# Performance work log

Measured on AMD Instinct MI355X. Metric: run time of the kernel, lower is better.

## Reference

```python
import jax, jax.numpy as jnp
import numpy as np
import math

D_MODEL = 1024
D_STATE = 128
EXPAND = 2
HEADDIM = 64
NGROUPS = 1
ROPE_FRACTION = 0.5
A_FLOOR = 1e-4
D_INNER = EXPAND * D_MODEL            # 2048
NHEADS = D_INNER // HEADDIM           # 32
SPLIT = int(D_STATE * ROPE_FRACTION)  # 64
R = SPLIT // 2                        # 32 rotary angles; rotary applied to first R state dims
D_IN_PROJ = 2 * D_INNER + 2 * D_STATE * NGROUPS + 3 * NHEADS + R  # 4480
BATCH = 1
SEQLEN = 1024


def setup_inputs() -> dict:
    key = jax.random.key(0)
    k0, k1, k2, k3 = jax.random.split(key, 4)
    u = jax.random.normal(k0, (BATCH, SEQLEN, D_MODEL), jnp.float32)
    w_in = jax.random.normal(k1, (D_IN_PROJ, D_MODEL), jnp.float32) * (D_MODEL ** -0.5)
    w_out = jax.random.normal(k2, (D_MODEL, D_INNER), jnp.float32) * (D_INNER ** -0.5)
    # dt_bias init matches torch: inverse-softplus of dt ~ LogUniform(dt_min, dt_max)
    dt = jnp.exp(jax.random.uniform(k3, (NHEADS,), jnp.float32)
                 * (math.log(0.1) - math.log(0.001)) + math.log(0.001))
    dt = jnp.maximum(dt, 1e-4)
    dt_bias = dt + jnp.log(-jnp.expm1(-dt))
    D = jnp.ones((NHEADS,), jnp.float32)
    return {"u": u, "w_in": w_in, "w_out": w_out, "dt_bias": dt_bias, "D": D}


def _mamba3_forward(u, w_in, w_out, dt_bias, D):
    b, l, _ = u.shape
    proj = u @ w_in.T  # [b, l, D_IN_PROJ]
    sizes = [D_INNER, D_INNER, D_STATE * NGROUPS, D_STATE * NGROUPS, NHEADS, NHEADS, NHEADS, R]
    idx = np.cumsum(sizes)[:-1]
    z, x, B, C, dd_dt, dd_A, trap, angles = jnp.split(proj, idx, axis=-1)

    A = jnp.minimum(-jax.nn.softplus(dd_A), -A_FLOOR)      # [b,l,h]
    dt = jax.nn.softplus(dd_dt + dt_bias)                  # [b,l,h]
    tr = jax.nn.sigmoid(trap)                              # [b,l,h]
    # rotary angle: tanh(angles)[b,l,1,R] * dt[b,l,h,1] * pi, cumsum over time
    theta = jnp.cumsum(jnp.tanh(angles)[:, :, None, :] * dt[..., None] * jnp.pi, axis=1)  # [b,l,h,R]

    x_h = x.reshape(b, l, NHEADS, HEADDIM)
    z_h = z.reshape(b, l, NHEADS, HEADDIM)
    B_h = B.reshape(b, l, NGROUPS, D_STATE)[:, :, 0, :]  # only group 0 is read in the loop
    C_h = C.reshape(b, l, NGROUPS, D_STATE)[:, :, 0, :]

    def step(carry, inp):
        sr, si, px = carry  # sr: [b,h,p,n], si: [b,h,p,R] (imag beyond R is identically zero)
        dt_t, A_t, tr_t, th, bt, ct, xt = inp
        alpha = jnp.exp(A_t * dt_t)[:, :, None, None]          # [b,h,1,1]
        beta = ((1.0 - tr_t) * dt_t)[:, :, None, None] * alpha
        gamma = (tr_t * dt_t)[:, :, None, None]
        base = bt[:, None, None, :] * (px[..., None] * beta + xt[..., None] * gamma)  # [b,h,p,n]
        rc = jnp.cos(th)[:, :, None, :]  # [b,h,1,R]
        rs = jnp.sin(th)[:, :, None, :]
        sr = sr * alpha + jnp.concatenate([base[..., :R] * rc, base[..., R:]], axis=-1)
        si = si * alpha + base[..., :R] * rs
        ctb = ct[:, None, None, :]
        y = (jnp.sum((sr[..., :R] * rc + si * rs) * ctb[..., :R], axis=-1)
             + jnp.sum(sr[..., R:] * ctb[..., R:], axis=-1))  # [b,h,p]
        return (sr, si, xt), y

    sr0 = jnp.zeros((b, NHEADS, HEADDIM, D_STATE), u.dtype)
    si0 = jnp.zeros((b, NHEADS, HEADDIM, R), u.dtype)
    px0 = jnp.zeros((b, NHEADS, HEADDIM), u.dtype)
    xs = (jnp.moveaxis(dt, 1, 0), jnp.moveaxis(A, 1, 0), jnp.moveaxis(tr, 1, 0),
          jnp.moveaxis(theta, 1, 0), jnp.moveaxis(B_h, 1, 0), jnp.moveaxis(C_h, 1, 0),
          jnp.moveaxis(x_h, 1, 0))
    _, ys = jax.lax.scan(step, (sr0, si0, px0), xs)  # [l,b,h,p]
    y = jnp.moveaxis(ys, 0, 1) + D[None, None, :, None] * x_h
    out = y * jax.nn.silu(z_h)
    return out.reshape(b, l, D_INNER) @ w_out.T


def reference(u, w_in, w_out, dt_bias, D):
    return _mamba3_forward(u, w_in, w_out, dt_bias, D)
```

## Files before the change

kernel.cpp:

```cpp
#include <hip/hip_runtime.h>
#include <math.h>

#define L_SEQ   1024
#define DMODEL  1024
#define DINNER  2048
#define NH      32
#define HD      64
#define NS      160
#define RR      32
#define NPROJ   4480
#define OFF_Z   0
#define OFF_X   2048
#define OFF_B   4096
#define OFF_C   4224
#define OFF_DT  4352
#define OFF_A   4384
#define OFF_TR  4416
#define OFF_ANG 4448
#define NC      16
#define CL      64
#define PIF     3.14159265358979323846f

typedef __attribute__((ext_vector_type(8))) short bf16x8;
typedef __attribute__((ext_vector_type(4))) float f32x4;
typedef unsigned int u32;
typedef unsigned short u16;

__device__ __forceinline__ float softplusf(float x) {
  return (x > 20.f) ? x : log1pf(expf(x));
}
__device__ __forceinline__ u16 f2bf(float f) {
  u32 u = __float_as_uint(f);
  u32 r = (u + 0x7FFFu + ((u >> 16) & 1u)) >> 16;
  return (u16)r;
}
__device__ __forceinline__ float bf2f(u16 v) {
  return __uint_as_float(((u32)v) << 16);
}

__device__ __forceinline__ void gload_lds16(const u16* g, u16* l) {
  __builtin_amdgcn_global_load_lds(
      (const __attribute__((address_space(1))) u32*)(unsigned long long)(const void*)g,
      (__attribute__((address_space(3))) u32*)(unsigned long long)(void*)l, 16, 0, 0);
}

__global__ __launch_bounds__(256) void cvt2_bf16(
    const float* __restrict__ s0, u16* __restrict__ d0, int q0,
    const float* __restrict__ s1, u16* __restrict__ d1, int q1) {
  int i = blockIdx.x * 256 + threadIdx.x;
  const float* s; u16* d; int j;
  if (i < q0) { s = s0; d = d0; j = i; }
  else { j = i - q0; if (j >= q1) return; s = s1; d = d1; }
  const float4* s4 = (const float4*)s;
  float4 a = s4[2 * j], b = s4[2 * j + 1];
  union { u16 h[8]; uint4 v; } o;
  o.h[0] = f2bf(a.x); o.h[1] = f2bf(a.y); o.h[2] = f2bf(a.z); o.h[3] = f2bf(a.w);
  o.h[4] = f2bf(b.x); o.h[5] = f2bf(b.y); o.h[6] = f2bf(b.z); o.h[7] = f2bf(b.w);
  ((uint4*)d)[j] = o.v;
}

template <int BM, int BN>
__global__ __launch_bounds__(256) void gemm_bf16(
    const u16* __restrict__ A, const u16* __restrict__ B,
    float* __restrict__ C, int N, int K) {
  constexpr int BK = 32;
  constexpr int WM = BM / 2, WN = BN / 2;
  constexpr int MF = WM / 16, NF = WN / 16;
  constexpr int CA = BM / 64;
  constexpr int CB = BN / 64;
  __shared__ u16 lds[(BM + BN) * BK];

  const int bm = blockIdx.y * BM, bn = blockIdx.x * BN;
  const int tid = threadIdx.x, w = tid >> 6, lane = tid & 63;
  const int wr = w >> 1, wc = w & 1;
  const int fr = lane & 15, sl = lane >> 4;
  const int lrow = lane >> 2, lslot = (lane & 3) * 8;

  const u16* gA[CA]; u16* lA[CA];
#pragma unroll
  for (int j = 0; j < CA; ++j) {
    int ca = w * CA + j;
    gA[j] = A + (size_t)(bm + ca * 16 + lrow) * K + lslot;
    lA[j] = lds + ca * 512;
  }
  const u16* gB[CB]; u16* lB[CB];
#pragma unroll
  for (int j = 0; j < CB; ++j) {
    int cb = w * CB + j;
    gB[j] = B + (size_t)(bn + cb * 16 + lrow) * K + lslot;
    lB[j] = lds + BM * 32 + cb * 512;
  }

  const u16* aptr[MF]; const u16* bptr[NF];
#pragma unroll
  for (int i = 0; i < MF; ++i)
    aptr[i] = lds + (wr * WM + i * 16 + fr) * 32 + sl * 8;
#pragma unroll
  for (int j = 0; j < NF; ++j)
    bptr[j] = lds + BM * 32 + (wc * WN + j * 16 + fr) * 32 + sl * 8;

  f32x4 acc[MF][NF] = {};
  const int iters = K / BK;

#pragma unroll
  for (int j = 0; j < CA; ++j) gload_lds16(gA[j], lA[j]);
#pragma unroll
  for (int j = 0; j < CB; ++j) gload_lds16(gB[j], lB[j]);

  for (int it = 0; it < iters; ++it) {
    __syncthreads();
    bf16x8 af[MF], bfv[NF];
#pragma unroll
    for (int i = 0; i < MF; ++i) af[i] = *(const bf16x8*)aptr[i];
#pragma unroll
    for (int j = 0; j < NF; ++j) bfv[j] = *(const bf16x8*)bptr[j];
    __syncthreads();
    if (it + 1 < iters) {
#pragma unroll
      for (int j = 0; j < CA; ++j) gload_lds16(gA[j] + (it + 1) * BK, lA[j]);
#pragma unroll
      for (int j = 0; j < CB; ++j) gload_lds16(gB[j] + (it + 1) * BK, lB[j]);
    }
#pragma unroll
    for (int i = 0; i < MF; ++i)
#pragma unroll
      for (int j = 0; j < NF; ++j)
        acc[i][j] = __builtin_amdgcn_mfma_f32_16x16x32_bf16(
            af[i], bfv[j], acc[i][j], 0, 0, 0);
  }

#pragma unroll
  for (int i = 0; i < MF; ++i) {
    int rb = bm + wr * WM + i * 16 + sl * 4;
#pragma unroll
    for (int j = 0; j < NF; ++j) {
      int cb = bn + wc * WN + j * 16 + fr;
#pragma unroll
      for (int r = 0; r < 4; ++r)
        C[(size_t)(rb + r) * N + cb] = acc[i][j][r];
    }
  }
}

__global__ __launch_bounds__(256) void prep_scalars_cvt(
    const float* __restrict__ proj, const float* __restrict__ dt_bias,
    float* __restrict__ dtA, float* __restrict__ lnaA,
    float* __restrict__ betaA, float* __restrict__ gammaA,
    float* __restrict__ angP,
    const float* __restrict__ wsrc, u16* __restrict__ wdst) {
  const int b = blockIdx.x;
  if (b < 1024) {
    int j = b * 256 + threadIdx.x;
    const float4* s4 = (const float4*)wsrc;
    float4 a = s4[2 * j], bb = s4[2 * j + 1];
    union { u16 h[8]; uint4 v; } o;
    o.h[0] = f2bf(a.x); o.h[1] = f2bf(a.y); o.h[2] = f2bf(a.z); o.h[3] = f2bf(a.w);
    o.h[4] = f2bf(bb.x); o.h[5] = f2bf(bb.y); o.h[6] = f2bf(bb.z); o.h[7] = f2bf(bb.w);
    ((uint4*)wdst)[j] = o.v;
    return;
  }
  int idx = (b - 1024) * 256 + threadIdx.x;
  int h = idx & 31, l = idx >> 5;
  const float* prow = proj + (size_t)l * NPROJ;
  float dt = softplusf(prow[OFF_DT + h] + dt_bias[h]);
  float Apos = fmaxf(softplusf(prow[OFF_A + h]), 1e-4f);
  float tr = 1.f / (1.f + expf(-prow[OFF_TR + h]));
  float lna = -Apos * dt;
  float alpha = expf(lna);
  dtA[idx] = dt;
  lnaA[idx] = lna;
  betaA[idx] = (1.f - tr) * dt * alpha;
  gammaA[idx] = tr * dt;
  angP[idx] = tanhf(prow[OFF_ANG + h]) * PIF;
}

__global__ __launch_bounds__(256) void theta_scan(
    const float* __restrict__ angP, const float* __restrict__ dtA,
    float* __restrict__ rc, float* __restrict__ rs) {
  const int h = blockIdx.x >> 5;
  const int r = blockIdx.x & 31;
  const int tid = threadIdx.x;
  __shared__ float ldssc[256];

  float csum[4];
  float run = 0.f;
#pragma unroll
  for (int i = 0; i < 4; ++i) {
    int l = tid * 4 + i;
    run += angP[l * NH + r] * dtA[l * NH + h];
    csum[i] = run;
  }
  ldssc[tid] = run;
  __syncthreads();
  for (int off = 1; off < 256; off <<= 1) {
    float t = (tid >= off) ? ldssc[tid - off] : 0.f;
    __syncthreads();
    ldssc[tid] += t;
    __syncthreads();
  }
  float excl = ldssc[tid] - run;
#pragma unroll
  for (int i = 0; i < 4; ++i) {
    int l = tid * 4 + i;
    float th = excl + csum[i];
    size_t o = ((size_t)l * NH + h) * RR + r;
    rc[o] = cosf(th);
    rs[o] = sinf(th);
  }
}

__global__ __launch_bounds__(256) void uvgA(
    const float* __restrict__ proj, const float* __restrict__ betaA,
    const float* __restrict__ gammaA, const float* __restrict__ lnaA,
    const float* __restrict__ rc, const float* __restrict__ rs,
    u16* __restrict__ U, u16* __restrict__ V, u16* __restrict__ Gt,
    float* __restrict__ cumA, float* __restrict__ adec,
    u16* __restrict__ S) {
  const int h = blockIdx.x >> 4, c = blockIdx.x & 15;
  const int c0 = c * CL;
  const int tid = threadIdx.x;
  const int w = tid >> 6, lane = tid & 63;

  __shared__ __attribute__((aligned(16))) char smem[54784];
  u16 (*Gw)[72]   = (u16(*)[72])(smem);
  float* wsc      = (float*)(smem + 9216);
  float* bet      = (float*)(smem + 9472);
  float* gam      = (float*)(smem + 9728);
  float (*xs)[64] = (float(*)[64])(smem + 10240);
  u16 (*Vl)[168]  = (u16(*)[168])(smem + 10240);
  u16 (*Vt)[72]   = (u16(*)[72])(smem + 31744);

  if (w < 3) {
    for (int i = tid; i < 65 * 16; i += 192) {
      int r = i >> 4, c4 = i & 15;
      int l = c0 - 1 + r;
      float4 v = {0.f, 0.f, 0.f, 0.f};
      if (l >= 0)
        v = *(const float4*)(proj + (size_t)l * NPROJ + OFF_X + h * HD + c4 * 4);
      *(float4*)&xs[r][c4 * 4] = v;
    }
  } else {
    const int t = lane;
    float v = lnaA[(c0 + t) * NH + h];
#pragma unroll
    for (int k = 1; k < 64; k <<= 1) {
      int src = t - k;
      float o = __shfl(v, src < 0 ? 0 : src);
      if (t >= k) v += o;
    }
    cumA[(size_t)h * L_SEQ + c0 + t] = v;
    if (t == 63) adec[h * NC + c] = expf(v);
    float c63 = __shfl(v, 63);
    wsc[t] = expf(c63 - v);
    bet[t] = betaA[(c0 + t) * NH + h];
    gam[t] = gammaA[(c0 + t) * NH + h];
  }
  __syncthreads();

  {
    const int p = lane;
    union { u16 hh[16]; uint4 q[2]; } og, ow;
    float xprev = xs[w * 16][p];
#pragma unroll
    for (int i = 0; i < 16; ++i) {
      int s = w * 16 + i;
      float xcur = xs[s + 1][p];
      float g = bet[s] * xprev + gam[s] * xcur;
      og.hh[i] = f2bf(g);
      ow.hh[i] = f2bf(g * wsc[s]);
      xprev = xcur;
    }
    uint4* gdst = (uint4*)(Gt + (((size_t)h * NC + c) * HD + p) * CL + w * 16);
    gdst[0] = og.q[0];
    gdst[1] = og.q[1];
    *(uint4*)&Gw[p][w * 16] = ow.q[0];
    *(uint4*)&Gw[p][w * 16 + 8] = ow.q[1];
  }
  __syncthreads();

  if (tid < 160) {
    const int n = tid;
    const int idxB = (n < 64) ? (n & 31) : (n - 32);
    const bool is_re = (n < 32);
    const bool has_rot = (n < 64);
    for (int ss = 0; ss < 64; ++ss) {
      int l = c0 + ss;
      const float* prow = proj + (size_t)l * NPROJ;
      float Bv = prow[OFF_B + idxB];
      float Cv = prow[OFF_C + idxB];
      if (has_rot) {
        float rv = is_re ? rc[((size_t)l * NH + h) * RR + idxB]
                         : rs[((size_t)l * NH + h) * RR + idxB];
        Bv *= rv; Cv *= rv;
      }
      u16 bb = f2bf(Bv);
      U[((size_t)h * L_SEQ + l) * NS + n] = f2bf(Cv);
      V[((size_t)h * L_SEQ + l) * NS + n] = bb;
      Vl[ss][n] = bb;
    }
  }
  __syncthreads();

  if (tid < 160) {
    int n = tid;
#pragma unroll
    for (int s2 = 0; s2 < 32; ++s2) {
      u32 lo = Vl[2 * s2][n], hi = Vl[2 * s2 + 1][n];
      *(u32*)&Vt[n][2 * s2] = lo | (hi << 16);
    }
  }
  __syncthreads();

  const int wr = w >> 1, wc = w & 1;
  const int fr = lane & 15, sl = lane >> 4;
  f32x4 acc[2][5] = {};
#pragma unroll
  for (int ks = 0; ks < 2; ++ks) {
    bf16x8 a0 = *(const bf16x8*)&Gw[wr * 32 + fr][ks * 32 + sl * 8];
    bf16x8 a1 = *(const bf16x8*)&Gw[wr * 32 + 16 + fr][ks * 32 + sl * 8];
    bf16x8 bv[5];
#pragma unroll
    for (int fj = 0; fj < 5; ++fj)
      bv[fj] = *(const bf16x8*)&Vt[wc * 80 + fj * 16 + fr][ks * 32 + sl * 8];
#pragma unroll
    for (int fj = 0; fj < 5; ++fj) {
      acc[0][fj] = __builtin_amdgcn_mfma_f32_16x16x32_bf16(a0, bv[fj], acc[0][fj], 0, 0, 0);
      acc[1][fj] = __builtin_amdgcn_mfma_f32_16x16x32_bf16(a1, bv[fj], acc[1][fj], 0, 0, 0);
    }
  }
  u16* Fb = S + (size_t)(c * NH + h) * HD * NS;
#pragma unroll
  for (int fi = 0; fi < 2; ++fi)
#pragma unroll
    for (int fj = 0; fj < 5; ++fj)
#pragma unroll
      for (int r = 0; r < 4; ++r) {
        int p = wr * 32 + fi * 16 + sl * 4 + r;
        int n = wc * 80 + fj * 16 + fr;
        Fb[(size_t)p * NS + n] = f2bf(acc[fi][fj][r]);
      }
}

__global__ __launch_bounds__(256) void combine(
    u16* __restrict__ S, const float* __restrict__ adec) {
  const int idx = blockIdx.x * 256 + threadIdx.x;
  if (idx >= NH * HD * NS) return;
  const int n = idx % NS;
  const int rem = idx / NS;
  const int p = rem & 63;
  const int h = rem >> 6;
  float F = 0.f;
  for (int c = 0; c < NC; ++c) {
    size_t off = ((size_t)(c * NH + h) * HD + p) * NS + n;
    float sv = bf2f(S[off]);
    S[off] = f2bf(F);
    F = fmaf(F, adec[h * NC + c], sv);
  }
}

__global__ __launch_bounds__(256) void passB(
    const float* __restrict__ proj, const u16* __restrict__ U,
    const u16* __restrict__ V, const u16* __restrict__ Gt,
    const float* __restrict__ cumA, const u16* __restrict__ S,
    const float* __restrict__ Dvec, u16* __restrict__ yz) {
  const int c = blockIdx.x >> 5, h = blockIdx.x & 31;
  const int c0 = c * CL;
  const int tid = threadIdx.x;
  const int w = tid >> 6, lane = tid & 63;
  const int wr = w >> 1, wc = w & 1;
  const int fr = lane & 15, sl = lane >> 4;
  __shared__ u16 Ul[64][168];
  __shared__ u16 BB[64][168];
  __shared__ u16 Ml[64][72];
  __shared__ u16 Gl[64][72];
  __shared__ float cums[64], ecum[64];

  const u16* Us = U + ((size_t)h * L_SEQ + c0) * NS;
  for (int i = tid; i < 1280; i += 256) {
    int r = i / 20, ch = i % 20;
    *(uint4*)&Ul[r][ch * 8] = *(const uint4*)(Us + (size_t)r * NS + ch * 8);
  }
  {
    const u16* S0 = S + (size_t)(c * NH + h) * HD * NS;
    for (int i = tid; i < 1280; i += 256) {
      int r = i / 20, ch = i % 20;
      *(uint4*)&BB[r][ch * 8] = *(const uint4*)(S0 + (size_t)r * NS + ch * 8);
    }
  }
  if (tid < 64) {
    float cv = cumA[(size_t)h * L_SEQ + c0 + tid];
    cums[tid] = cv;
    ecum[tid] = expf(cv);
  }
  __syncthreads();

  f32x4 acc[2][2] = {};
#pragma unroll
  for (int ks = 0; ks < 5; ++ks) {
    bf16x8 a0 = *(const bf16x8*)&Ul[wr * 32 + fr][ks * 32 + sl * 8];
    bf16x8 a1 = *(const bf16x8*)&Ul[wr * 32 + 16 + fr][ks * 32 + sl * 8];
    bf16x8 b0 = *(const bf16x8*)&BB[wc * 32 + fr][ks * 32 + sl * 8];
    bf16x8 b1 = *(const bf16x8*)&BB[wc * 32 + 16 + fr][ks * 32 + sl * 8];
    acc[0][0] = __builtin_amdgcn_mfma_f32_16x16x32_bf16(a0, b0, acc[0][0], 0, 0, 0);
    acc[0][1] = __builtin_amdgcn_mfma_f32_16x16x32_bf16(a0, b1, acc[0][1], 0, 0, 0);
    acc[1][0] = __builtin_amdgcn_mfma_f32_16x16x32_bf16(a1, b0, acc[1][0], 0, 0, 0);
    acc[1][1] = __builtin_amdgcn_mfma_f32_16x16x32_bf16(a1, b1, acc[1][1], 0, 0, 0);
  }
#pragma unroll
  for (int fi = 0; fi < 2; ++fi)
#pragma unroll
    for (int fj = 0; fj < 2; ++fj)
#pragma unroll
      for (int r = 0; r < 4; ++r)
        acc[fi][fj][r] *= ecum[wr * 32 + fi * 16 + sl * 4 + r];
  __syncthreads();

  const u16* Vs = V + ((size_t)h * L_SEQ + c0) * NS;
  for (int i = tid; i < 1280; i += 256) {
    int r = i / 20, ch = i % 20;
    *(uint4*)&BB[r][ch * 8] = *(const uint4*)(Vs + (size_t)r * NS + ch * 8);
  }
  const u16* Gs = Gt + ((size_t)h * NC + c) * HD * CL;
  for (int i = tid; i < 512; i += 256) {
    int p = i >> 3, ch = i & 7;
    *(uint4*)&Gl[p][ch * 8] = *(const uint4*)(Gs + (size_t)p * CL + ch * 8);
  }
  __syncthreads();

  f32x4 pac[2][2] = {};
#pragma unroll
  for (int ks = 0; ks < 5; ++ks) {
    bf16x8 a0 = *(const bf16x8*)&Ul[wr * 32 + fr][ks * 32 + sl * 8];
    bf16x8 a1 = *(const bf16x8*)&Ul[wr * 32 + 16 + fr][ks * 32 + sl * 8];
    bf16x8 b0 = *(const bf16x8*)&BB[wc * 32 + fr][ks * 32 + sl * 8];
    bf16x8 b1 = *(const bf16x8*)&BB[wc * 32 + 16 + fr][ks * 32 + sl * 8];
    pac[0][0] = __builtin_amdgcn_mfma_f32_16x16x32_bf16(a0, b0, pac[0][0], 0, 0, 0);
    pac[0][1] = __builtin_amdgcn_mfma_f32_16x16x32_bf16(a0, b1, pac[0][1], 0, 0, 0);
    pac[1][0] = __builtin_amdgcn_mfma_f32_16x16x32_bf16(a1, b0, pac[1][0], 0, 0, 0);
    pac[1][1] = __builtin_amdgcn_mfma_f32_16x16x32_bf16(a1, b1, pac[1][1], 0, 0, 0);
  }
#pragma unroll
  for (int fi = 0; fi < 2; ++fi)
#pragma unroll
    for (int fj = 0; fj < 2; ++fj)
#pragma unroll
      for (int r = 0; r < 4; ++r) {
        int t = wr * 32 + fi * 16 + sl * 4 + r;
        int ss = wc * 32 + fj * 16 + fr;
        float m = (ss <= t) ? expf(cums[t] - cums[ss]) * pac[fi][fj][r] : 0.f;
        Ml[t][ss] = f2bf(m);
      }
  __syncthreads();

#pragma unroll
  for (int ks = 0; ks < 2; ++ks) {
    bf16x8 a0 = *(const bf16x8*)&Ml[wr * 32 + fr][ks * 32 + sl * 8];
    bf16x8 a1 = *(const bf16x8*)&Ml[wr * 32 + 16 + fr][ks * 32 + sl * 8];
    bf16x8 b0 = *(const bf16x8*)&Gl[wc * 32 + fr][ks * 32 + sl * 8];
    bf16x8 b1 = *(const bf16x8*)&Gl[wc * 32 + 16 + fr][ks * 32 + sl * 8];
    acc[0][0] = __builtin_amdgcn_mfma_f32_16x16x32_bf16(a0, b0, acc[0][0], 0, 0, 0);
    acc[0][1] = __builtin_amdgcn_mfma_f32_16x16x32_bf16(a0, b1, acc[0][1], 0, 0, 0);
    acc[1][0] = __builtin_amdgcn_mfma_f32_16x16x32_bf16(a1, b0, acc[1][0], 0, 0, 0);
    acc[1][1] = __builtin_amdgcn_mfma_f32_16x16x32_bf16(a1, b1, acc[1][1], 0, 0, 0);
  }

  const float Dh = Dvec[h];
#pragma unroll
  for (int fi = 0; fi < 2; ++fi)
#pragma unroll
    for (int fj = 0; fj < 2; ++fj)
#pragma unroll
      for (int r = 0; r < 4; ++r) {
        int t = wr * 32 + fi * 16 + sl * 4 + r;
        int p = wc * 32 + fj * 16 + fr;
        int l = c0 + t;
        float x = proj[(size_t)l * NPROJ + OFF_X + h * HD + p];
        float z = proj[(size_t)l * NPROJ + OFF_Z + h * HD + p];
        float y = acc[fi][fj][r] + Dh * x;
        float sg = z / (1.f + expf(-z));
        yz[(size_t)l * DINNER + h * HD + p] = f2bf(y * sg);
      }
}

extern "C" void kernel_launch(void* const* d_in, const int* in_sizes, int n_in,
                              void* d_out, int out_size, void* d_ws, size_t ws_size,
                              hipStream_t stream) {
  const float* u       = (const float*)d_in[0];
  const float* w_in    = (const float*)d_in[1];
  const float* w_out   = (const float*)d_in[2];
  const float* dt_bias = (const float*)d_in[3];
  const float* Dvec    = (const float*)d_in[4];
  float* out = (float*)d_out;

  float* ws = (float*)d_ws;
  float* proj   = ws;
  float* dtA    = proj + 4587520;
  float* lnaA   = dtA + 32768;
  float* betaA  = lnaA + 32768;
  float* gammaA = betaA + 32768;
  float* cumA   = gammaA + 32768;
  float* adec   = cumA + 32768;
  float* angP   = adec + 512;
  float* rcb    = angP + 32768;
  float* rsb    = rcb + 1048576;
  u16*   Sb     = (u16*)(rsb + 1048576);
  u16*   Gtb    = Sb + 5242880;
  u16*   Ubuf   = Gtb + 2097152;
  u16*   Vbuf   = Ubuf + 5242880;
  u16*   yzb    = Vbuf + 5242880;
  u16*   wob    = yzb + 2097152;
  u16*   ub     = Ubuf;
  u16*   wib    = Ubuf + 1048576;

  cvt2_bf16<<<(131072 + 573440) / 256, 256, 0, stream>>>(
      u, ub, 131072, w_in, wib, 573440);

  gemm_bf16<128, 128><<<dim3(NPROJ / 128, L_SEQ / 128), 256, 0, stream>>>(
      ub, wib, proj, NPROJ, DMODEL);

  prep_scalars_cvt<<<1024 + 128, 256, 0, stream>>>(
      proj, dt_bias, dtA, lnaA, betaA, gammaA, angP, w_out, wob);

  theta_scan<<<NH * RR, 256, 0, stream>>>(angP, dtA, rcb, rsb);

  uvgA<<<NH * NC, 256, 0, stream>>>(
      proj, betaA, gammaA, lnaA, rcb, rsb, Ubuf, Vbuf, Gtb, cumA, adec, Sb);

  combine<<<(NH * HD * NS + 255) / 256, 256, 0, stream>>>(Sb, adec);

  passB<<<NC * NH, 256, 0, stream>>>(
      proj, Ubuf, Vbuf, Gtb, cumA, Sb, Dvec, yzb);

  gemm_bf16<64, 64><<<dim3(DMODEL / 64, L_SEQ / 64), 256, 0, stream>>>(
      yzb, wob, out, DMODEL, DINNER);
}
```

Before: 133.9 us.

## Fuse scan pipeline into one persistent kernel with software grid barriers

Merges prep_scalars, theta_scan, uvgA, combine and passB into a single 512-block persistent kernel separated by atomic-based grid barriers. The w_out bf16 conversion moves into the initial conversion kernel, and the bf16 copies of u and w_in are relocated into the S buffer. This removes several kernel launch gaps and tail effects. The cost is barrier spin overhead, and correctness depends on all 512 blocks being co-resident, which launch_bounds(256,2) is meant to help.

```diff
diff --git a/kernel.cpp b/kernel.cpp
--- a/kernel.cpp
+++ b/kernel.cpp
@@ -44,13 +44,34 @@
       (__attribute__((address_space(3))) u32*)(unsigned long long)(void*)l, 16, 0, 0);
 }
 
-__global__ __launch_bounds__(256) void cvt2_bf16(
-    const float* __restrict__ s0, u16* __restrict__ d0, int q0,
-    const float* __restrict__ s1, u16* __restrict__ d1, int q1) {
+__device__ __forceinline__ void grid_bar(u32* bar) {
+  __syncthreads();
+  if (threadIdx.x == 0) {
+    __threadfence();
+    u32 gen = __hip_atomic_load(bar + 1, __ATOMIC_RELAXED, __HIP_MEMORY_SCOPE_AGENT);
+    u32 arr = __hip_atomic_fetch_add(bar, 1u, __ATOMIC_ACQ_REL, __HIP_MEMORY_SCOPE_AGENT);
+    if (arr + 1u == gridDim.x) {
+      __hip_atomic_store(bar, 0u, __ATOMIC_RELAXED, __HIP_MEMORY_SCOPE_AGENT);
+      __hip_atomic_store(bar + 1, gen + 1u, __ATOMIC_RELEASE, __HIP_MEMORY_SCOPE_AGENT);
+    } else {
+      while (__hip_atomic_load(bar + 1, __ATOMIC_ACQUIRE, __HIP_MEMORY_SCOPE_AGENT) == gen)
+        __builtin_amdgcn_s_sleep(2);
+    }
+    __threadfence();
+  }
+  __syncthreads();
+}
+
+__global__ __launch_bounds__(256) void cvt3(
+    const float* __restrict__ s0, u16* __restrict__ d0,
+    const float* __restrict__ s1, u16* __restrict__ d1,
+    const float* __restrict__ s2, u16* __restrict__ d2) {
   int i = blockIdx.x * 256 + threadIdx.x;
   const float* s; u16* d; int j;
-  if (i < q0) { s = s0; d = d0; j = i; }
-  else { j = i - q0; if (j >= q1) return; s = s1; d = d1; }
+  if (i < 131072)      { s = s0; d = d0; j = i; }
+  else if (i < 704512) { s = s1; d = d1; j = i - 131072; }
+  else if (i < 966656) { s = s2; d = d2; j = i - 704512; }
+  else return;
   const float4* s4 = (const float4*)s;
   float4 a = s4[2 * j], b = s4[2 * j + 1];
   union { u16 h[8]; uint4 v; } o;
@@ -142,344 +163,329 @@
   }
 }
 
-__global__ __launch_bounds__(256) void prep_scalars_cvt(
+__global__ __launch_bounds__(256, 2) void mega(
     const float* __restrict__ proj, const float* __restrict__ dt_bias,
+    const float* __restrict__ Dvec,
     float* __restrict__ dtA, float* __restrict__ lnaA,
     float* __restrict__ betaA, float* __restrict__ gammaA,
-    float* __restrict__ angP,
-    const float* __restrict__ wsrc, u16* __restrict__ wdst) {
-  const int b = blockIdx.x;
-  if (b < 1024) {
-    int j = b * 256 + threadIdx.x;
-    const float4* s4 = (const float4*)wsrc;
-    float4 a = s4[2 * j], bb = s4[2 * j + 1];
-    union { u16 h[8]; uint4 v; } o;
-    o.h[0] = f2bf(a.x); o.h[1] = f2bf(a.y); o.h[2] = f2bf(a.z); o.h[3] = f2bf(a.w);
-    o.h[4] = f2bf(bb.x); o.h[5] = f2bf(bb.y); o.h[6] = f2bf(bb.z); o.h[7] = f2bf(bb.w);
-    ((uint4*)wdst)[j] = o.v;
-    return;
-  }
-  int idx = (b - 1024) * 256 + threadIdx.x;
-  int h = idx & 31, l = idx >> 5;
-  const float* prow = proj + (size_t)l * NPROJ;
-  float dt = softplusf(prow[OFF_DT + h] + dt_bias[h]);
-  float Apos = fmaxf(softplusf(prow[OFF_A + h]), 1e-4f);
-  float tr = 1.f / (1.f + expf(-prow[OFF_TR + h]));
-  float lna = -Apos * dt;
-  float alpha = expf(lna);
-  dtA[idx] = dt;
-  lnaA[idx] = lna;
-  betaA[idx] = (1.f - tr) * dt * alpha;
-  gammaA[idx] = tr * dt;
-  angP[idx] = tanhf(prow[OFF_ANG + h]) * PIF;
-}
-
-__global__ __launch_bounds__(256) void theta_scan(
-    const float* __restrict__ angP, const float* __restrict__ dtA,
-    float* __restrict__ rc, float* __restrict__ rs) {
-  const int h = blockIdx.x >> 5;
-  const int r = blockIdx.x & 31;
-  const int tid = threadIdx.x;
-  __shared__ float ldssc[256];
-
-  float csum[4];
-  float run = 0.f;
-#pragma unroll
-  for (int i = 0; i < 4; ++i) {
-    int l = tid * 4 + i;
-    run += angP[l * NH + r] * dtA[l * NH + h];
-    csum[i] = run;
-  }
-  ldssc[tid] = run;
-  __syncthreads();
-  for (int off = 1; off < 256; off <<= 1) {
-    float t = (tid >= off) ? ldssc[tid - off] : 0.f;
-    __syncthreads();
-    ldssc[tid] += t;
-    __syncthreads();
-  }
-  float excl = ldssc[tid] - run;
-#pragma unroll
-  for (int i = 0; i < 4; ++i) {
-    int l = tid * 4 + i;
-    float th = excl + csum[i];
-    size_t o = ((size_t)l * NH + h) * RR + r;
-    rc[o] = cosf(th);
-    rs[o] = sinf(th);
-  }
-}
-
-__global__ __launch_bounds__(256) void uvgA(
-    const float* __restrict__ proj, const float* __restrict__ betaA,
-    const float* __restrict__ gammaA, const float* __restrict__ lnaA,
-    const float* __restrict__ rc, const float* __restrict__ rs,
-    u16* __restrict__ U, u16* __restrict__ V, u16* __restrict__ Gt,
     float* __restrict__ cumA, float* __restrict__ adec,
-    u16* __restrict__ S) {
-  const int h = blockIdx.x >> 4, c = blockIdx.x & 15;
-  const int c0 = c * CL;
-  const int tid = threadIdx.x;
-  const int w = tid >> 6, lane = tid & 63;
-
-  __shared__ __attribute__((aligned(16))) char smem[54784];
-  u16 (*Gw)[72]   = (u16(*)[72])(smem);
-  float* wsc      = (float*)(smem + 9216);
-  float* bet      = (float*)(smem + 9472);
-  float* gam      = (float*)(smem + 9728);
-  float (*xs)[64] = (float(*)[64])(smem + 10240);
-  u16 (*Vl)[168]  = (u16(*)[168])(smem + 10240);
-  u16 (*Vt)[72]   = (u16(*)[72])(smem + 31744);
-
-  if (w < 3) {
-    for (int i = tid; i < 65 * 16; i += 192) {
-      int r = i >> 4, c4 = i & 15;
-      int l = c0 - 1 + r;
-      float4 v = {0.f, 0.f, 0.f, 0.f};
-      if (l >= 0)
-        v = *(const float4*)(proj + (size_t)l * NPROJ + OFF_X + h * HD + c4 * 4);
-      *(float4*)&xs[r][c4 * 4] = v;
-    }
-  } else {
-    const int t = lane;
-    float v = lnaA[(c0 + t) * NH + h];
-#pragma unroll
-    for (int k = 1; k < 64; k <<= 1) {
-      int src = t - k;
-      float o = __shfl(v, src < 0 ? 0 : src);
-      if (t >= k) v += o;
-    }
-    cumA[(size_t)h * L_SEQ + c0 + t] = v;
-    if (t == 63) adec[h * NC + c] = expf(v);
-    float c63 = __shfl(v, 63);
-    wsc[t] = expf(c63 - v);
-    bet[t] = betaA[(c0 + t) * NH + h];
-    gam[t] = gammaA[(c0 + t) * NH + h];
-  }
-  __syncthreads();
-
-  {
-    const int p = lane;
-    union { u16 hh[16]; uint4 q[2]; } og, ow;
-    float xprev = xs[w * 16][p];
-#pragma unroll
-    for (int i = 0; i < 16; ++i) {
-      int s = w * 16 + i;
-      float xcur = xs[s + 1][p];
-      float g = bet[s] * xprev + gam[s] * xcur;
-      og.hh[i] = f2bf(g);
-      ow.hh[i] = f2bf(g * wsc[s]);
-      xprev = xcur;
-    }
-    uint4* gdst = (uint4*)(Gt + (((size_t)h * NC + c) * HD + p) * CL + w * 16);
-    gdst[0] = og.q[0];
-    gdst[1] = og.q[1];
-    *(uint4*)&Gw[p][w * 16] = ow.q[0];
-    *(uint4*)&Gw[p][w * 16 + 8] = ow.q[1];
-  }
-  __syncthreads();
-
-  if (tid < 160) {
-    const int n = tid;
-    const int idxB = (n < 64) ? (n & 31) : (n - 32);
-    const bool is_re = (n < 32);
-    const bool has_rot = (n < 64);
-    for (int ss = 0; ss < 64; ++ss) {
-      int l = c0 + ss;
-      const float* prow = proj + (size_t)l * NPROJ;
-      float Bv = prow[OFF_B + idxB];
-      float Cv = prow[OFF_C + idxB];
-      if (has_rot) {
-        float rv = is_re ? rc[((size_t)l * NH + h) * RR + idxB]
-                         : rs[((size_t)l * NH + h) * RR + idxB];
-        Bv *= rv; Cv *= rv;
-      }
-      u16 bb = f2bf(Bv);
-      U[((size_t)h * L_SEQ + l) * NS + n] = f2bf(Cv);
-      V[((size_t)h * L_SEQ + l) * NS + n] = bb;
-      Vl[ss][n] = bb;
-    }
-  }
-  __syncthreads();
-
-  if (tid < 160) {
-    int n = tid;
-#pragma unroll
-    for (int s2 = 0; s2 < 32; ++s2) {
-      u32 lo = Vl[2 * s2][n], hi = Vl[2 * s2 + 1][n];
-      *(u32*)&Vt[n][2 * s2] = lo | (hi << 16);
-    }
-  }
-  __syncthreads();
-
-  const int wr = w >> 1, wc = w & 1;
-  const int fr = lane & 15, sl = lane >> 4;
-  f32x4 acc[2][5] = {};
-#pragma unroll
-  for (int ks = 0; ks < 2; ++ks) {
-    bf16x8 a0 = *(const bf16x8*)&Gw[wr * 32 + fr][ks * 32 + sl * 8];
-    bf16x8 a1 = *(const bf16x8*)&Gw[wr * 32 + 16 + fr][ks * 32 + sl * 8];
-    bf16x8 bv[5];
-#pragma unroll
-    for (int fj = 0; fj < 5; ++fj)
-      bv[fj] = *(const bf16x8*)&Vt[wc * 80 + fj * 16 + fr][ks * 32 + sl * 8];
-#pragma unroll
-    for (int fj = 0; fj < 5; ++fj) {
-      acc[0][fj] = __builtin_amdgcn_mfma_f32_16x16x32_bf16(a0, bv[fj], acc[0][fj], 0, 0, 0);
-      acc[1][fj] = __builtin_amdgcn_mfma_f32_16x16x32_bf16(a1, bv[fj], acc[1][fj], 0, 0, 0);
-    }
-  }
-  u16* Fb = S + (size_t)(c * NH + h) * HD * NS;
-#pragma unroll
-  for (int fi = 0; fi < 2; ++fi)
-#pragma unroll
-    for (int fj = 0; fj < 5; ++fj)
-#pragma unroll
-      for (int r = 0; r < 4; ++r) {
-        int p = wr * 32 + fi * 16 + sl * 4 + r;
-        int n = wc * 80 + fj * 16 + fr;
-        Fb[(size_t)p * NS + n] = f2bf(acc[fi][fj][r]);
-      }
-}
-
-__global__ __launch_bounds__(256) void combine(
-    u16* __restrict__ S, const float* __restrict__ adec) {
-  const int idx = blockIdx.x * 256 + threadIdx.x;
-  if (idx >= NH * HD * NS) return;
-  const int n = idx % NS;
-  const int rem = idx / NS;
-  const int p = rem & 63;
-  const int h = rem >> 6;
-  float F = 0.f;
-  for (int c = 0; c < NC; ++c) {
-    size_t off = ((size_t)(c * NH + h) * HD + p) * NS + n;
-    float sv = bf2f(S[off]);
-    S[off] = f2bf(F);
-    F = fmaf(F, adec[h * NC + c], sv);
-  }
-}
-
-__global__ __launch_bounds__(256) void passB(
-    const float* __restrict__ proj, const u16* __restrict__ U,
-    const u16* __restrict__ V, const u16* __restrict__ Gt,
-    const float* __restrict__ cumA, const u16* __restrict__ S,
-    const float* __restrict__ Dvec, u16* __restrict__ yz) {
-  const int c = blockIdx.x >> 5, h = blockIdx.x & 31;
-  const int c0 = c * CL;
+    float* __restrict__ angP, float* __restrict__ rcb, float* __restrict__ rsb,
+    u16* __restrict__ Sb, u16* __restrict__ Gtb,
+    u16* __restrict__ Ubuf, u16* __restrict__ Vbuf,
+    u16* __restrict__ yzb, u32* bar) {
+  const int bid = blockIdx.x;
   const int tid = threadIdx.x;
   const int w = tid >> 6, lane = tid & 63;
   const int wr = w >> 1, wc = w & 1;
   const int fr = lane & 15, sl = lane >> 4;
-  __shared__ u16 Ul[64][168];
-  __shared__ u16 BB[64][168];
-  __shared__ u16 Ml[64][72];
-  __shared__ u16 Gl[64][72];
-  __shared__ float cums[64], ecum[64];
-
-  const u16* Us = U + ((size_t)h * L_SEQ + c0) * NS;
-  for (int i = tid; i < 1280; i += 256) {
-    int r = i / 20, ch = i % 20;
-    *(uint4*)&Ul[r][ch * 8] = *(const uint4*)(Us + (size_t)r * NS + ch * 8);
-  }
+
+  __shared__ __attribute__((aligned(16))) char smem[61952];
+
+  if (tid < 64) {
+    int idx = bid * 64 + tid;
+    int h = idx & 31, l = idx >> 5;
+    const float* prow = proj + (size_t)l * NPROJ;
+    float dt = softplusf(prow[OFF_DT + h] + dt_bias[h]);
+    float Apos = fmaxf(softplusf(prow[OFF_A + h]), 1e-4f);
+    float tr = 1.f / (1.f + expf(-prow[OFF_TR + h]));
+    float lna = -Apos * dt;
+    float alpha = expf(lna);
+    dtA[idx] = dt;
+    lnaA[idx] = lna;
+    betaA[idx] = (1.f - tr) * dt * alpha;
+    gammaA[idx] = tr * dt;
+    angP[idx] = tanhf(prow[OFF_ANG + h]) * PIF;
+  }
+  grid_bar(bar);
+
   {
-    const u16* S0 = S + (size_t)(c * NH + h) * HD * NS;
+    float* ldssc = (float*)smem;
+    for (int cc = 0; cc < 2; ++cc) {
+      int ch = bid * 2 + cc;
+      int h = ch >> 5, r = ch & 31;
+      float csum[4];
+      float run = 0.f;
+#pragma unroll
+      for (int i = 0; i < 4; ++i) {
+        int l = tid * 4 + i;
+        run += angP[l * NH + r] * dtA[l * NH + h];
+        csum[i] = run;
+      }
+      ldssc[tid] = run;
+      __syncthreads();
+      for (int off = 1; off < 256; off <<= 1) {
+        float t = (tid >= off) ? ldssc[tid - off] : 0.f;
+        __syncthreads();
+        ldssc[tid] += t;
+        __syncthreads();
+      }
+      float excl = ldssc[tid] - run;
+#pragma unroll
+      for (int i = 0; i < 4; ++i) {
+        int l = tid * 4 + i;
+        float th = excl + csum[i];
+        size_t o = ((size_t)l * NH + h) * RR + r;
+        rcb[o] = cosf(th);
+        rsb[o] = sinf(th);
+      }
+      __syncthreads();
+    }
+  }
+  grid_bar(bar);
+
+  {
+    const int h = bid >> 4, c = bid & 15;
+    const int c0 = c * CL;
+    u16 (*Gw)[72]   = (u16(*)[72])(smem);
+    float* wsc      = (float*)(smem + 9216);
+    float* bet      = (float*)(smem + 9472);
+    float* gam      = (float*)(smem + 9728);
+    float (*xs)[64] = (float(*)[64])(smem + 10240);
+    u16 (*Vl)[168]  = (u16(*)[168])(smem + 10240);
+    u16 (*Vt)[72]   = (u16(*)[72])(smem + 31744);
+
+    if (w < 3) {
+      for (int i = tid; i < 65 * 16; i += 192) {
+        int r = i >> 4, c4 = i & 15;
+        int l = c0 - 1 + r;
+        float4 v = {0.f, 0.f, 0.f, 0.f};
+        if (l >= 0)
+          v = *(const float4*)(proj + (size_t)l * NPROJ + OFF_X + h * HD + c4 * 4);
+        *(float4*)&xs[r][c4 * 4] = v;
+      }
+    } else {
+      const int t = lane;
+      float v = lnaA[(c0 + t) * NH + h];
+#pragma unroll
+      for (int k = 1; k < 64; k <<= 1) {
+        int src = t - k;
+        float o = __shfl(v, src < 0 ? 0 : src);
+        if (t >= k) v += o;
+      }
+      cumA[(size_t)h * L_SEQ + c0 + t] = v;
+      if (t == 63) adec[h * NC + c] = expf(v);
+      float c63 = __shfl(v, 63);
+      wsc[t] = expf(c63 - v);
+      bet[t] = betaA[(c0 + t) * NH + h];
+      gam[t] = gammaA[(c0 + t) * NH + h];
+    }
+    __syncthreads();
+
+    {
+      const int p = lane;
+      union { u16 hh[16]; uint4 q[2]; } og, ow;
+      float xprev = xs[w * 16][p];
+#pragma unroll
+      for (int i = 0; i < 16; ++i) {
+        int s = w * 16 + i;
+        float xcur = xs[s + 1][p];
+        float g = bet[s] * xprev + gam[s] * xcur;
+        og.hh[i] = f2bf(g);
+        ow.hh[i] = f2bf(g * wsc[s]);
+        xprev = xcur;
+      }
+      uint4* gdst = (uint4*)(Gtb + (((size_t)h * NC + c) * HD + p) * CL + w * 16);
+      gdst[0] = og.q[0];
+      gdst[1] = og.q[1];
+      *(uint4*)&Gw[p][w * 16] = ow.q[0];
+      *(uint4*)&Gw[p][w * 16 + 8] = ow.q[1];
+    }
+    __syncthreads();
+
+    if (tid < 160) {
+      const int n = tid;
+      const int idxB = (n < 64) ? (n & 31) : (n - 32);
+      const bool is_re = (n < 32);
+      const bool has_rot = (n < 64);
+      for (int ss = 0; ss < 64; ++ss) {
+        int l = c0 + ss;
+        const float* prow = proj + (size_t)l * NPROJ;
+        float Bv = prow[OFF_B + idxB];
+        float Cv = prow[OFF_C + idxB];
+        if (has_rot) {
+          float rv = is_re ? rcb[((size_t)l * NH + h) * RR + idxB]
+                           : rsb[((size_t)l * NH + h) * RR + idxB];
+          Bv *= rv; Cv *= rv;
+        }
+        u16 bb = f2bf(Bv);
+        Ubuf[((size_t)h * L_SEQ + l) * NS + n] = f2bf(Cv);
+        Vbuf[((size_t)h * L_SEQ + l) * NS + n] = bb;
+        Vl[ss][n] = bb;
+      }
+    }
+    __syncthreads();
+
+    if (tid < 160) {
+      int n = tid;
+#pragma unroll
+      for (int s2 = 0; s2 < 32; ++s2) {
+        u32 lo = Vl[2 * s2][n], hi = Vl[2 * s2 + 1][n];
+        *(u32*)&Vt[n][2 * s2] = lo | (hi << 16);
+      }
+    }
+    __syncthreads();
+
+    f32x4 acc[2][5] = {};
+#pragma unroll
+    for (int ks = 0; ks < 2; ++ks) {
+      bf16x8 a0 = *(const bf16x8*)&Gw[wr * 32 + fr][ks * 32 + sl * 8];
+      bf16x8 a1 = *(const bf16x8*)&Gw[wr * 32 + 16 + fr][ks * 32 + sl * 8];
+      bf16x8 bv[5];
+#pragma unroll
+      for (int fj = 0; fj < 5; ++fj)
+        bv[fj] = *(const bf16x8*)&Vt[wc * 80 + fj * 16 + fr][ks * 32 + sl * 8];
+#pragma unroll
+      for (int fj = 0; fj < 5; ++fj) {
+        acc[0][fj] = __builtin_amdgcn_mfma_f32_16x16x32_bf16(a0, bv[fj], acc[0][fj], 0, 0, 0);
+        acc[1][fj] = __builtin_amdgcn_mfma_f32_16x16x32_bf16(a1, bv[fj], acc[1][fj], 0, 0, 0);
+      }
+    }
+    u16* Fb = Sb + (size_t)(c * NH + h) * HD * NS;
+#pragma unroll
+    for (int fi = 0; fi < 2; ++fi)
+#pragma unroll
+      for (int fj = 0; fj < 5; ++fj)
+#pragma unroll
+        for (int r = 0; r < 4; ++r) {
+          int p = wr * 32 + fi * 16 + sl * 4 + r;
+          int n = wc * 80 + fj * 16 + fr;
+          Fb[(size_t)p * NS + n] = f2bf(acc[fi][fj][r]);
+        }
+  }
+  grid_bar(bar);
+
+  for (int i = tid; i < 640; i += 256) {
+    int idx = bid * 640 + i;
+    int n = idx % NS;
+    int rem = idx / NS;
+    int p = rem & 63;
+    int h = rem >> 6;
+    float F = 0.f;
+    for (int c = 0; c < NC; ++c) {
+      size_t off = ((size_t)(c * NH + h) * HD + p) * NS + n;
+      float sv = bf2f(Sb[off]);
+      Sb[off] = f2bf(F);
+      F = fmaf(F, adec[h * NC + c], sv);
+    }
+  }
+  grid_bar(bar);
+
+  {
+    const int c = bid >> 5, h = bid & 31;
+    const int c0 = c * CL;
+    u16 (*Ul)[168] = (u16(*)[168])(smem);
+    u16 (*BB)[168] = (u16(*)[168])(smem + 21504);
+    u16 (*Ml)[72]  = (u16(*)[72]) (smem + 43008);
+    u16 (*Gl)[72]  = (u16(*)[72]) (smem + 52224);
+    float* cums = (float*)(smem + 61440);
+    float* ecum = (float*)(smem + 61696);
+
+    const u16* Us = Ubuf + ((size_t)h * L_SEQ + c0) * NS;
     for (int i = tid; i < 1280; i += 256) {
       int r = i / 20, ch = i % 20;
-      *(uint4*)&BB[r][ch * 8] = *(const uint4*)(S0 + (size_t)r * NS + ch * 8);
-    }
-  }
-  if (tid < 64) {
-    float cv = cumA[(size_t)h * L_SEQ + c0 + tid];
-    cums[tid] = cv;
-    ecum[tid] = expf(cv);
-  }
-  __syncthreads();
-
-  f32x4 acc[2][2] = {};
-#pragma unroll
-  for (int ks = 0; ks < 5; ++ks) {
-    bf16x8 a0 = *(const bf16x8*)&Ul[wr * 32 + fr][ks * 32 + sl * 8];
-    bf16x8 a1 = *(const bf16x8*)&Ul[wr * 32 + 16 + fr][ks * 32 + sl * 8];
-    bf16x8 b0 = *(const bf16x8*)&BB[wc * 32 + fr][ks * 32 + sl * 8];
-    bf16x8 b1 = *(const bf16x8*)&BB[wc * 32 + 16 + fr][ks * 32 + sl * 8];
-    acc[0][0] = __builtin_amdgcn_mfma_f32_16x16x32_bf16(a0, b0, acc[0][0], 0, 0, 0);
-    acc[0][1] = __builtin_amdgcn_mfma_f32_16x16x32_bf16(a0, b1, acc[0][1], 0, 0, 0);
-    acc[1][0] = __builtin_amdgcn_mfma_f32_16x16x32_bf16(a1, b0, acc[1][0], 0, 0, 0);
-    acc[1][1] = __builtin_amdgcn_mfma_f32_16x16x32_bf16(a1, b1, acc[1][1], 0, 0, 0);
-  }
-#pragma unroll
-  for (int fi = 0; fi < 2; ++fi)
-#pragma unroll
-    for (int fj = 0; fj < 2; ++fj)
-#pragma unroll
-      for (int r = 0; r < 4; ++r)
-        acc[fi][fj][r] *= ecum[wr * 32 + fi * 16 + sl * 4 + r];
-  __syncthreads();
-
-  const u16* Vs = V + ((size_t)h * L_SEQ + c0) * NS;
-  for (int i = tid; i < 1280; i += 256) {
-    int r = i / 20, ch = i % 20;
-    *(uint4*)&BB[r][ch * 8] = *(const uint4*)(Vs + (size_t)r * NS + ch * 8);
-  }
-  const u16* Gs = Gt + ((size_t)h * NC + c) * HD * CL;
-  for (int i = tid; i < 512; i += 256) {
-    int p = i >> 3, ch = i & 7;
-    *(uint4*)&Gl[p][ch * 8] = *(const uint4*)(Gs + (size_t)p * CL + ch * 8);
-  }
-  __syncthreads();
-
-  f32x4 pac[2][2] = {};
-#pragma unroll
-  for (int ks = 0; ks < 5; ++ks) {
-    bf16x8 a0 = *(const bf16x8*)&Ul[wr * 32 + fr][ks * 32 + sl * 8];
-    bf16x8 a1 = *(const bf16x8*)&Ul[wr * 32 + 16 + fr][ks * 32 + sl * 8];
-    bf16x8 b0 = *(const bf16x8*)&BB[wc * 32 + fr][ks * 32 + sl * 8];
-    bf16x8 b1 = *(const bf16x8*)&BB[wc * 32 + 16 + fr][ks * 32 + sl * 8];
-    pac[0][0] = __builtin_amdgcn_mfma_f32_16x16x32_bf16(a0, b0, pac[0][0], 0, 0, 0);
-    pac[0][1] = __builtin_amdgcn_mfma_f32_16x16x32_bf16(a0, b1, pac[0][1], 0, 0, 0);
-    pac[1][0] = __builtin_amdgcn_mfma_f32_16x16x32_bf16(a1, b0, pac[1][0], 0, 0, 0);
-    pac[1][1] = __builtin_amdgcn_mfma_f32_16x16x32_bf16(a1, b1, pac[1][1], 0, 0, 0);
-  }
-#pragma unroll
-  for (int fi = 0; fi < 2; ++fi)
-#pragma unroll
-    for (int fj = 0; fj < 2; ++fj)
-#pragma unroll
-      for (int r = 0; r < 4; ++r) {
-        int t = wr * 32 + fi * 16 + sl * 4 + r;
-        int ss = wc * 32 + fj * 16 + fr;
-        float m = (ss <= t) ? expf(cums[t] - cums[ss]) * pac[fi][fj][r] : 0.f;
-        Ml[t][ss] = f2bf(m);
-      }
-  __syncthreads();
-
-#pragma unroll
-  for (int ks = 0; ks < 2; ++ks) {
-    bf16x8 a0 = *(const bf16x8*)&Ml[wr * 32 + fr][ks * 32 + sl * 8];
-    bf16x8 a1 = *(const bf16x8*)&Ml[wr * 32 + 16 + fr][ks * 32 + sl * 8];
-    bf16x8 b0 = *(const bf16x8*)&Gl[wc * 32 + fr][ks * 32 + sl * 8];
-    bf16x8 b1 = *(const bf16x8*)&Gl[wc * 32 + 16 + fr][ks * 32 + sl * 8];
-    acc[0][0] = __builtin_amdgcn_mfma_f32_16x16x32_bf16(a0, b0, acc[0][0], 0, 0, 0);
-    acc[0][1] = __builtin_amdgcn_mfma_f32_16x16x32_bf16(a0, b1, acc[0][1], 0, 0, 0);
-    acc[1][0] = __builtin_amdgcn_mfma_f32_16x16x32_bf16(a1, b0, acc[1][0], 0, 0, 0);
-    acc[1][1] = __builtin_amdgcn_mfma_f32_16x16x32_bf16(a1, b1, acc[1][1], 0, 0, 0);
-  }
-
-  const float Dh = Dvec[h];
-#pragma unroll
-  for (int fi = 0; fi < 2; ++fi)
-#pragma unroll
-    for (int fj = 0; fj < 2; ++fj)
-#pragma unroll
-      for (int r = 0; r < 4; ++r) {
-        int t = wr * 32 + fi * 16 + sl * 4 + r;
-        int p = wc * 32 + fj * 16 + fr;
-        int l = c0 + t;
-        float x = proj[(size_t)l * NPROJ + OFF_X + h * HD + p];
-        float z = proj[(size_t)l * NPROJ + OFF_Z + h * HD + p];
-        float y = acc[fi][fj][r] + Dh * x;
-        float sg = z / (1.f + expf(-z));
-        yz[(size_t)l * DINNER + h * HD + p] = f2bf(y * sg);
-      }
+      *(uint4*)&Ul[r][ch * 8] = *(const uint4*)(Us + (size_t)r * NS + ch * 8);
+    }
+    {
+      const u16* S0 = Sb + (size_t)(c * NH + h) * HD * NS;
+      for (int i = tid; i < 1280; i += 256) {
+        int r = i / 20, ch = i % 20;
+        *(uint4*)&BB[r][ch * 8] = *(const uint4*)(S0 + (size_t)r * NS + ch * 8);
+      }
+    }
+    if (tid < 64) {
+      float cv = cumA[(size_t)h * L_SEQ + c0 + tid];
+      cums[tid] = cv;
+      ecum[tid] = expf(cv);
+    }
+    __syncthreads();
+
+    f32x4 acc[2][2] = {};
+#pragma unroll
+    for (int ks = 0; ks < 5; ++ks) {
+      bf16x8 a0 = *(const bf16x8*)&Ul[wr * 32 + fr][ks * 32 + sl * 8];
+      bf16x8 a1 = *(const bf16x8*)&Ul[wr * 32 + 16 + fr][ks * 32 + sl * 8];
+      bf16x8 b0 = *(const bf16x8*)&BB[wc * 32 + fr][ks * 32 + sl * 8];
+      bf16x8 b1 = *(const bf16x8*)&BB[wc * 32 + 16 + fr][ks * 32 + sl * 8];
+      acc[0][0] = __builtin_amdgcn_mfma_f32_16x16x32_bf16(a0, b0, acc[0][0], 0, 0, 0);
+      acc[0][1] = __builtin_amdgcn_mfma_f32_16x16x32_bf16(a0, b1, acc[0][1], 0, 0, 0);
+      acc[1][0] = __builtin_amdgcn_mfma_f32_16x16x32_bf16(a1, b0, acc[1][0], 0, 0, 0);
+      acc[1][1] = __builtin_amdgcn_mfma_f32_16x16x32_bf16(a1, b1, acc[1][1], 0, 0, 0);
+    }
+#pragma unroll
+    for (int fi = 0; fi < 2; ++fi)
+#pragma unroll
+      for (int fj = 0; fj < 2; ++fj)
+#pragma unroll
+        for (int r = 0; r < 4; ++r)
+          acc[fi][fj][r] *= ecum[wr * 32 + fi * 16 + sl * 4 + r];
+    __syncthreads();
+
+    const u16* Vs = Vbuf + ((size_t)h * L_SEQ + c0) * NS;
+    for (int i = tid; i < 1280; i += 256) {
+      int r = i / 20, ch = i % 20;
+      *(uint4*)&BB[r][ch * 8] = *(const uint4*)(Vs + (size_t)r * NS + ch * 8);
+    }
+    const u16* Gs = Gtb + ((size_t)h * NC + c) * HD * CL;
+    for (int i = tid; i < 512; i += 256) {
+      int p = i >> 3, ch = i & 7;
+      *(uint4*)&Gl[p][ch * 8] = *(const uint4*)(Gs + (size_t)p * CL + ch * 8);
+    }
+    __syncthreads();
+
+    f32x4 pac[2][2] = {};
+#pragma unroll
+    for (int ks = 0; ks < 5; ++ks) {
+      bf16x8 a0 = *(const bf16x8*)&Ul[wr * 32 + fr][ks * 32 + sl * 8];
+      bf16x8 a1 = *(const bf16x8*)&Ul[wr * 32 + 16 + fr][ks * 32 + sl * 8];
+      bf16x8 b0 = *(const bf16x8*)&BB[wc * 32 + fr][ks * 32 + sl * 8];
+      bf16x8 b1 = *(const bf16x8*)&BB[wc * 32 + 16 + fr][ks * 32 + sl * 8];
+      pac[0][0] = __builtin_amdgcn_mfma_f32_16x16x32_bf16(a0, b0, pac[0][0], 0, 0, 0);
+      pac[0][1] = __builtin_amdgcn_mfma_f32_16x16x32_bf16(a0, b1, pac[0][1], 0, 0, 0);
+      pac[1][0] = __builtin_amdgcn_mfma_f32_16x16x32_bf16(a1, b0, pac[1][0], 0, 0, 0);
+      pac[1][1] = __builtin_amdgcn_mfma_f32_16x16x32_bf16(a1, b1, pac[1][1], 0, 0, 0);
+    }
+#pragma unroll
+    for (int fi = 0; fi < 2; ++fi)
+#pragma unroll
+      for (int fj = 0; fj < 2; ++fj)
+#pragma unroll
+        for (int r = 0; r < 4; ++r) {
+          int t = wr * 32 + fi * 16 + sl * 4 + r;
+          int ss = wc * 32 + fj * 16 + fr;
+          float m = (ss <= t) ? expf(cums[t] - cums[ss]) * pac[fi][fj][r] : 0.f;
+          Ml[t][ss] = f2bf(m);
+        }
+    __syncthreads();
+
+#pragma unroll
+    for (int ks = 0; ks < 2; ++ks) {
+      bf16x8 a0 = *(const bf16x8*)&Ml[wr * 32 + fr][ks * 32 + sl * 8];
+      bf16x8 a1 = *(const bf16x8*)&Ml[wr * 32 + 16 + fr][ks * 32 + sl * 8];
+      bf16x8 b0 = *(const bf16x8*)&Gl[wc * 32 + fr][ks * 32 + sl * 8];
+      bf16x8 b1 = *(const bf16x8*)&Gl[wc * 32 + 16 + fr][ks * 32 + sl * 8];
+      acc[0][0] = __builtin_amdgcn_mfma_f32_16x16x32_bf16(a0, b0, acc[0][0], 0, 0, 0);
+      acc[0][1] = __builtin_amdgcn_mfma_f32_16x16x32_bf16(a0, b1, acc[0][1], 0, 0, 0);
+      acc[1][0] = __builtin_amdgcn_mfma_f32_16x16x32_bf16(a1, b0, acc[1][0], 0, 0, 0);
+      acc[1][1] = __builtin_amdgcn_mfma_f32_16x16x32_bf16(a1, b1, acc[1][1], 0, 0, 0);
+    }
+
+    const float Dh = Dvec[h];
+#pragma unroll
+    for (int fi = 0; fi < 2; ++fi)
+#pragma unroll
+      for (int fj = 0; fj < 2; ++fj)
+#pragma unroll
+        for (int r = 0; r < 4; ++r) {
+          int t = wr * 32 + fi * 16 + sl * 4 + r;
+          int p = wc * 32 + fj * 16 + fr;
+          int l = c0 + t;
+          float x = proj[(size_t)l * NPROJ + OFF_X + h * HD + p];
+          float z = proj[(size_t)l * NPROJ + OFF_Z + h * HD + p];
+          float y = acc[fi][fj][r] + Dh * x;
+          float sg = z / (1.f + expf(-z));
+          yzb[(size_t)l * DINNER + h * HD + p] = f2bf(y * sg);
+        }
+  }
 }
 
 extern "C" void kernel_launch(void* const* d_in, const int* in_sizes, int n_in,
@@ -509,27 +515,20 @@
   u16*   Vbuf   = Ubuf + 5242880;
   u16*   yzb    = Vbuf + 5242880;
   u16*   wob    = yzb + 2097152;
-  u16*   ub     = Ubuf;
-  u16*   wib    = Ubuf + 1048576;
-
-  cvt2_bf16<<<(131072 + 573440) / 256, 256, 0, stream>>>(
-      u, ub, 131072, w_in, wib, 573440);
+  u32*   bar    = (u32*)(wob + 2097152);
+  u16*   ub     = Sb;
+  u16*   wib    = Sb + 1048576;
+
+  hipMemsetAsync(bar, 0, 8, stream);
+
+  cvt3<<<3776, 256, 0, stream>>>(u, ub, w_in, wib, w_out, wob);
 
   gemm_bf16<128, 128><<<dim3(NPROJ / 128, L_SEQ / 128), 256, 0, stream>>>(
       ub, wib, proj, NPROJ, DMODEL);
 
-  prep_scalars_cvt<<<1024 + 128, 256, 0, stream>>>(
-      proj, dt_bias, dtA, lnaA, betaA, gammaA, angP, w_out, wob);
-
-  theta_scan<<<NH * RR, 256, 0, stream>>>(angP, dtA, rcb, rsb);
-
-  uvgA<<<NH * NC, 256, 0, stream>>>(
-      proj, betaA, gammaA, lnaA, rcb, rsb, Ubuf, Vbuf, Gtb, cumA, adec, Sb);
-
-  combine<<<(NH * HD * NS + 255) / 256, 256, 0, stream>>>(Sb, adec);
-
-  passB<<<NC * NH, 256, 0, stream>>>(
-      proj, Ubuf, Vbuf, Gtb, cumA, Sb, Dvec, yzb);
+  mega<<<512, 256, 0, stream>>>(
+      proj, dt_bias, Dvec, dtA, lnaA, betaA, gammaA, cumA, adec,
+      angP, rcb, rsb, Sb, Gtb, Ubuf, Vbuf, yzb, bar);
 
   gemm_bf16<64, 64><<<dim3(DMODEL / 64, L_SEQ / 64), 256, 0, stream>>>(
       yzb, wob, out, DMODEL, DINNER);
```

Result: slower. 491.2 us (+266.7%).
